# Kernel tuning notes

Hardware: AMD Instinct MI355X
Metric: run time of the kernel (lower is better)

Reference implementation:

```python
import jax, jax.numpy as jnp
import numpy as np

N_F, N_T = 211, 390
PAD_T, PAD_F = 2 * N_T, N_F  # zero_pad = (780, 211): right pad in time, bottom pad in freq
N_FILTS = 119
COCH_RESCALE = 100.0
CLAMP_MIN = 1e-8


def setup_inputs() -> dict:
    key = jax.random.key(0)
    k1, k2, k3 = jax.random.split(key, 3)
    x = jax.random.uniform(k1, (1, 1, N_F, N_T), dtype=jnp.float32)
    Ht_real = jax.random.normal(k2, (N_FILTS, N_F + PAD_F, N_T + PAD_T), dtype=jnp.float32)
    Ht_imag = jax.random.normal(k3, (N_FILTS, N_F + PAD_F, N_T + PAD_T), dtype=jnp.float32)
    return {"x": x, "Ht_real": Ht_real, "Ht_imag": Ht_imag}


def reference(x, Ht_real, Ht_imag):
    # x: [B, 1, N_F, N_T] cochleagram
    xs = x[:, 0] * COCH_RESCALE  # squeeze channel, rescale -> [B, N_F, N_T]
    # ConstantPad2d((0, PAD_T, 0, PAD_F)): pad time on the right, freq on the bottom
    xp = jnp.pad(xs, ((0, 0), (0, PAD_F), (0, PAD_T)))  # [B, 422, 1170]
    X = jnp.fft.fft2(xp)  # full (two-sided) 2D FFT, complex64
    H = Ht_real + 1j * Ht_imag  # [F, 422, 1170]
    Y = X[:, None, :, :] * H[None]  # broadcast complex multiply -> [B, F, 422, 1170]
    y = jnp.fft.ifft2(Y)
    real = jnp.real(y[:, :, :N_F, :N_T])  # crop to [B, F, 211, 390]
    power = jnp.clip(real * real, CLAMP_MIN)  # SquareReal with clamp min
    # AdaptiveAvgPool2d((1,1)) -> mean over freq/time, keep dims
    out = jnp.mean(power, axis=(-2, -1), keepdims=True)  # [B, F, 1, 1]
    return out
```

## Files before the change

kernel.cpp:

```cpp
#include <hip/hip_runtime.h>
#include <math.h>

constexpr int NF  = 119;
constexpr int D1  = 422;
constexpr int D2  = 1170;

constexpr int OFF_W390  = 0;
constexpr int OFF_T1170 = 390;
constexpr int OFF_W512  = 1560;
constexpr int OFF_CHIRP = 2072;
constexpr int OFF_U422  = 2283;
constexpr int OFF_BF    = 2494;
constexpr int OFF_T422  = 3006;

constexpr int KP1 = 2368;
constexpr int KB1 = KP1 * 2;
constexpr int ZS2 = 784;
constexpr int KP2 = 448;
constexpr int KB2 = KP2 * 2;

constexpr float SC_A   = 9.765625e-4f;
constexpr double S_D   = 1024.0 / (422.0 * 1170.0);
constexpr float TH_CL  = (float)(1e-8 / (S_D * S_D));
constexpr float FINAL  = (float)(S_D * S_D / (211.0 * 390.0));

typedef _Float16 h16;
typedef _Float16 h16x2 __attribute__((ext_vector_type(2)));
typedef _Float16 h16x8 __attribute__((ext_vector_type(8)));
typedef float f32x4 __attribute__((ext_vector_type(4)));

__device__ inline float2 cmul(float2 a, float2 b) {
  return make_float2(fmaf(a.x, b.x, -(a.y * b.y)), fmaf(a.x, b.y, a.y * b.x));
}
__device__ inline float2 cmulc(float2 a, float2 b) {
  return make_float2(fmaf(a.x, b.x, (a.y * b.y)), fmaf(a.y, b.x, -(a.x * b.y)));
}
__device__ inline void cfma(float2& c, float2 a, float2 b) {
  c.x = fmaf(a.x, b.x, fmaf(-a.y, b.y, c.x));
  c.y = fmaf(a.x, b.y, fmaf(a.y, b.x, c.y));
}

__device__ inline void async16(const void* g, void* l) {
  __builtin_amdgcn_global_load_lds((const __attribute__((address_space(1))) unsigned int*)g,
                                   (__attribute__((address_space(3))) unsigned int*)l, 16, 0, 0);
}

__device__ inline void fft512_lds(float2* a, const float2* w, int lt, int inv) {
  #pragma unroll
  for (int s = 0; s < 2; ++s) {
    int i = lt + (s << 8);
    int j = (int)(__brev((unsigned)i) >> 23);
    if (j > i) { float2 t = a[i]; a[i] = a[j]; a[j] = t; }
  }
  __syncthreads();
  for (int s = 1; s <= 9; ++s) {
    int half = 1 << (s - 1);
    int pos = lt & (half - 1);
    int grp = lt >> (s - 1);
    int i = (grp << s) + pos;
    int j = i + half;
    float2 tw = w[pos << (9 - s)];
    if (inv) tw.y = -tw.y;
    float2 t = cmul(a[j], tw);
    float2 ai = a[i];
    a[j] = make_float2(ai.x - t.x, ai.y - t.y);
    a[i] = make_float2(ai.x + t.x, ai.y + t.y);
    __syncthreads();
  }
}

__device__ inline void bluestein_core(float2* buf, const float2* w512s, const float2* __restrict__ Bt, int lt) {
  __syncthreads();
  fft512_lds(buf, w512s, lt, 0);
  #pragma unroll
  for (int s = 0; s < 2; ++s) { int i = lt + (s << 8); buf[i] = cmul(buf[i], Bt[i]); }
  __syncthreads();
  fft512_lds(buf, w512s, lt, 1);
}

template <int INV>
__device__ inline void dft390x3(const float2* a0, const float2* a1, const float2* a2,
                                float2* b0, float2* b1, float2* b2,
                                const float2* w, int tid,
                                float2& X0, float2& X1, float2& X2) {
  bool act = tid < 390;
  if (act) {
    int ka = tid % 30, nb = tid / 30;
    float2 c0 = make_float2(0.f, 0.f), c1 = c0, c2 = c0;
    int idx = 0, step = 13 * ka;
    #pragma unroll 6
    for (int na = 0; na < 30; ++na) {
      float2 tw = w[idx];
      if (INV) tw.y = -tw.y;
      int src = 13 * na + nb;
      cfma(c0, a0[src], tw);
      cfma(c1, a1[src], tw);
      cfma(c2, a2[src], tw);
      idx += step; if (idx >= 390) idx -= 390;
    }
    float2 t2 = w[nb * ka];
    if (INV) t2.y = -t2.y;
    int o = ka * 13 + nb;
    b0[o] = cmul(c0, t2);
    b1[o] = cmul(c1, t2);
    b2[o] = cmul(c2, t2);
  }
  __syncthreads();
  if (act) {
    int ka = tid % 30, kb = tid / 30;
    float2 c0 = make_float2(0.f, 0.f), c1 = c0, c2 = c0;
    int idx = 0, step = 30 * kb;
    #pragma unroll
    for (int nb = 0; nb < 13; ++nb) {
      float2 tw = w[idx];
      if (INV) tw.y = -tw.y;
      int src = ka * 13 + nb;
      cfma(c0, b0[src], tw);
      cfma(c1, b1[src], tw);
      cfma(c2, b2[src], tw);
      idx += step; if (idx >= 390) idx -= 390;
    }
    X0 = c0; X1 = c1; X2 = c2;
  }
  __syncthreads();
}


__global__ __launch_bounds__(512) void k_init(float2* __restrict__ tab, float* __restrict__ out) {
  int tid = threadIdx.x;
  __shared__ float2 bufE[512], bufO[512];
  __shared__ float2 w512s[512];
  __shared__ float2 chirps[211];
  const double PI = 3.14159265358979323846;
  for (int j = tid; j < 390; j += 512) {
    double a = -2.0 * PI * (double)j / 390.0; double s, c; sincos(a, &s, &c);
    tab[OFF_W390 + j] = make_float2((float)c, (float)s);
  }
  for (int j = tid; j < 1170; j += 512) {
    double a = 2.0 * PI * (double)j / 1170.0; double s, c; sincos(a, &s, &c);
    tab[OFF_T1170 + j] = make_float2((float)c, (float)s);
  }
  for (int j = tid; j < 422; j += 512) {
    double a = 2.0 * PI * (double)j / 422.0; double s, c; sincos(a, &s, &c);
    tab[OFF_T422 + j] = make_float2((float)c, (float)s);
  }
  for (int j = tid; j < 512; j += 512) {
    double a = -2.0 * PI * (double)j / 512.0; double s, c; sincos(a, &s, &c);
    float2 v = make_float2((float)c, (float)s);
    tab[OFF_W512 + j] = v; w512s[j] = v;
  }
  for (int n = tid; n < 211; n += 512) {
    int m = (n * n) % 422;
    double a = PI * (double)m / 211.0; double s, c; sincos(a, &s, &c);
    float2 v = make_float2((float)c, (float)s);
    tab[OFF_CHIRP + n] = v; chirps[n] = v;
  }
  for (int p = tid; p < 211; p += 512) {
    double a = 2.0 * PI * (double)p / 422.0; double s, c; sincos(a, &s, &c);
    tab[OFF_U422 + p] = make_float2((float)c, (float)s);
  }
  if (tid < NF) out[tid] = 0.0f;
  __syncthreads();
  int g = tid >> 8, lt = tid & 255;
  float2* buf = g ? bufO : bufE;
  #pragma unroll
  for (int s = 0; s < 2; ++s) {
    int i = lt + (s << 8);
    float2 v = make_float2(0.f, 0.f);
    if (i < 211) v = chirps[i];
    else if (i >= 302) v = chirps[512 - i];
    buf[i] = v;
  }
  __syncthreads();
  fft512_lds(buf, w512s, lt, 0);
  const float sc = 1.0f / 512.0f;
  if (g == 0) {
    #pragma unroll
    for (int s = 0; s < 2; ++s) {
      int i = lt + (s << 8);
      float2 v = buf[i];
      v.x *= sc; v.y *= sc;
      tab[OFF_BF + i] = v;
    }
  }
}

__global__ __launch_bounds__(256) void k_buildB(const float2* __restrict__ tab, h16* __restrict__ B1t) {
  int n = blockIdx.x;
  int q = n >> 1, c = n & 1;
  int tid = threadIdx.x;
  __shared__ float2 t[1170];
  for (int j = tid; j < 1170; j += 256) t[j] = tab[OFF_T1170 + j];
  __syncthreads();
  h16* row = B1t + (size_t)n * KP1;
  for (int k2 = tid; k2 < 1184; k2 += 256) {
    h16x2 h;
    if (k2 < 1170) {
      unsigned m = ((unsigned)q * (unsigned)k2) % 1170u;
      float2 e = t[m];
      h.x = (h16)(c ? e.y : e.x);
      h.y = (h16)(c ? e.x : -e.y);
    } else { h.x = (h16)0.f; h.y = (h16)0.f; }
    *(h16x2*)(row + 2 * k2) = h;
  }
}

__global__ __launch_bounds__(256) void k_buildA2(const float2* __restrict__ tab, h16* __restrict__ A2) {
  int p = blockIdx.x;
  int tid = threadIdx.x;
  __shared__ float2 t[422];
  for (int j = tid; j < 422; j += 256) t[j] = tab[OFF_T422 + j];
  __syncthreads();
  h16* row = A2 + (size_t)p * KP2;
  for (int k1 = tid; k1 < 224; k1 += 256) {
    h16x2 h; h.x = (h16)0.f; h.y = (h16)0.f;
    if (k1 < 212) {
      unsigned m = ((unsigned)p * (unsigned)k1) % 422u;
      float2 e = t[m];
      float cf = (k1 == 0 || k1 == 211) ? 1.f : 2.f;
      h.x = (h16)(cf * e.x);
      h.y = (h16)(-cf * e.y);
    }
    *(h16x2*)(row + 2 * k1) = h;
  }
}

__global__ __launch_bounds__(448) void k_rowfft(const float* __restrict__ x, const float2* __restrict__ tab,
                                                float2* __restrict__ X) {
  int i = blockIdx.x;
  int tid = threadIdx.x;
  __shared__ float2 a0[390], a1[390], a2[390], b0[390], b1[390], b2[390];
  __shared__ float2 w390s[390];
  __shared__ float2 t1170s[780];
  for (int j = tid; j < 390; j += 448) w390s[j] = tab[OFF_W390 + j];
  for (int j = tid; j < 780; j += 448) t1170s[j] = tab[OFF_T1170 + j];
  __syncthreads();
  for (int j = tid; j < 390; j += 448) {
    float xv = 100.0f * x[i * 390 + j];
    a0[j] = make_float2(xv, 0.0f);
    float2 t1 = t1170s[j];
    a1[j] = make_float2(xv * t1.x, -xv * t1.y);
    float2 t2 = t1170s[2 * j];
    a2[j] = make_float2(xv * t2.x, -xv * t2.y);
  }
  __syncthreads();
  float2 X0 = make_float2(0,0), X1 = X0, X2 = X0;
  dft390x3<0>(a0, a1, a2, b0, b1, b2, w390s, tid, X0, X1, X2);
  if (tid < 390) {
    size_t base = (size_t)i * D2 + 3 * (size_t)tid;
    X[base + 0] = X0; X[base + 1] = X1; X[base + 2] = X2;
  }
}

__global__ __launch_bounds__(512) void k_colfft(const float2* __restrict__ tab, float2* __restrict__ X) {
  int tid = threadIdx.x;
  int q0 = blockIdx.x * 8;
  int ncols = min(8, D2 - q0);
  __shared__ float Xre[8][212], Xim[8][212];
  __shared__ float2 bufE[512], bufO[512];
  __shared__ float2 w512s[512], chirps[211], u422s[211];
  for (int j = tid; j < 512; j += 512) w512s[j] = tab[OFF_W512 + j];
  for (int j = tid; j < 211; j += 512) { chirps[j] = tab[OFF_CHIRP + j]; u422s[j] = tab[OFF_U422 + j]; }
  const float2* Bf = tab + OFF_BF;
  for (int idx = tid; idx < 211 * 8; idx += 512) {
    int i = idx >> 3, c = idx & 7;
    float2 v = make_float2(0.f, 0.f);
    if (c < ncols) v = X[(size_t)i * D2 + q0 + c];
    Xre[c][i] = v.x; Xim[c][i] = v.y;
  }
  __syncthreads();
  int g = tid >> 8, lt = tid & 255;
  float2* buf = g ? bufO : bufE;
  for (int c = 0; c < ncols; ++c) {
    #pragma unroll
    for (int s = 0; s < 2; ++s) {
      int i2 = lt + (s << 8);
      float2 v = make_float2(0.f, 0.f);
      if (i2 < 211) {
        v = make_float2(Xre[c][i2], Xim[c][i2]);
        if (g) v = cmulc(v, u422s[i2]);
        v = cmulc(v, chirps[i2]);
      }
      buf[i2] = v;
    }
    bluestein_core(buf, w512s, Bf, lt);
    #pragma unroll
    for (int s = 0; s < 2; ++s) {
      int i2 = lt + (s << 8);
      if (i2 < 211) {
        float2 r = cmulc(buf[i2], chirps[i2]);
        X[(size_t)(2 * i2 + g) * D2 + q0 + c] = r;
      }
    }
    __syncthreads();
  }
}

__global__ __launch_bounds__(256) void k_buildA(const float* __restrict__ Hr, const float* __restrict__ Hi,
                                                const float2* __restrict__ X, h16* __restrict__ A, int f0) {
  int k1 = blockIdx.x, fl = blockIdx.y, f = f0 + fl;
  int tid = threadIdx.x;
  int m1 = (422 - k1) % 422;
  size_t hb  = (size_t)f * (D1 * D2) + (size_t)k1 * D2;
  size_t hmb = (size_t)f * (D1 * D2) + (size_t)m1 * D2;
  const float2* Xr = X + (size_t)k1 * D2;
  h16* Arow = A + ((size_t)fl * 212 + k1) * KP1;
  for (int k2 = tid; k2 < 1170; k2 += 256) {
    int rk = k2 ? 1170 - k2 : 0;
    float gr = 0.5f * (Hr[hb + k2] + Hr[hmb + rk]);
    float gi = 0.5f * (Hi[hb + k2] - Hi[hmb + rk]);
    float2 xv = Xr[k2];
    float yr = (xv.x * gr - xv.y * gi) * SC_A;
    float yi = (xv.x * gi + xv.y * gr) * SC_A;
    h16x2 h; h.x = (h16)yr; h.y = (h16)yi;
    *(h16x2*)(Arow + 2 * k2) = h;
  }
  if (tid < 28) Arow[2340 + tid] = (h16)0.f;
}

__global__ __launch_bounds__(256) void k_gemm1(const h16* __restrict__ A, const h16* __restrict__ B1t,
                                               h16* __restrict__ Z) {
  int fl = blockIdx.y;
  int mt = blockIdx.x / 7, nt = blockIdx.x % 7;
  const int M0 = mt ? 84 : 0;
  const int N0 = (nt == 6) ? 652 : nt * 128;
  int tid = threadIdx.x, wv = tid >> 6, ln = tid & 63;
  int l15 = ln & 15, l16 = ln >> 4;
  int wm = (wv >> 1) * 64, wn = (wv & 1) * 64;
  __shared__ __align__(16) h16 Alds[128 * 32];
  __shared__ __align__(16) h16 Blds[128 * 32];
  const char* Ag = (const char*)(A + (size_t)fl * 212 * KP1);
  const char* Bg = (const char*)B1t;
  f32x4 acc[4][4] = {};
  for (int kc = 0; kc < 74; ++kc) {
    int kb = kc * 64;
    __syncthreads();
    #pragma unroll
    for (int s = 0; s < 2; ++s) {
      int L = ((wv * 2 + s) * 64 + ln) * 16;
      int row = L >> 6, colb = L & 63;
      async16(Ag + (size_t)(M0 + row) * KB1 + kb + colb, (char*)Alds + (wv * 2 + s) * 1024);
      async16(Bg + (size_t)(N0 + row) * KB1 + kb + colb, (char*)Blds + (wv * 2 + s) * 1024);
    }
    __syncthreads();
    h16x8 af[4], bf[4];
    const h16x8* Av = (const h16x8*)Alds;
    const h16x8* Bv = (const h16x8*)Blds;
    #pragma unroll
    for (int i = 0; i < 4; ++i) af[i] = Av[(wm + i * 16 + l15) * 4 + l16];
    #pragma unroll
    for (int j = 0; j < 4; ++j) bf[j] = Bv[(wn + j * 16 + l15) * 4 + l16];
    #pragma unroll
    for (int i = 0; i < 4; ++i)
      #pragma unroll
      for (int j = 0; j < 4; ++j)
        acc[i][j] = __builtin_amdgcn_mfma_f32_16x16x32_f16(af[i], bf[j], acc[i][j], 0, 0, 0);
  }
  h16* Zf = Z + (size_t)fl * 212 * ZS2;
  #pragma unroll
  for (int i = 0; i < 4; ++i) {
    #pragma unroll
    for (int j = 0; j < 4; ++j) {
      #pragma unroll
      for (int r = 0; r < 4; ++r) {
        int m = M0 + wm + i * 16 + l16 * 4 + r;
        int n = N0 + wn + j * 16 + l15;
        Zf[(size_t)m * ZS2 + n] = (h16)acc[i][j][r];
      }
    }
  }
}

__global__ __launch_bounds__(256) void k_gemm2(const h16* __restrict__ A2, const h16* __restrict__ Z,
                                               float* __restrict__ out, int f0) {
  int fl = blockIdx.y, f = f0 + fl;
  int mt = blockIdx.x / 7, nt = blockIdx.x % 7;
  const int M0 = (mt == 3) ? 147 : mt * 64;
  const int pmin = (mt == 3) ? 192 : 0;
  const int N0 = (nt == 6) ? 326 : nt * 64;
  const int qmin = (nt == 6) ? 384 : 0;
  int tid = threadIdx.x, wv = tid >> 6, ln = tid & 63;
  int l15 = ln & 15, l16 = ln >> 4;
  int wm = (wv >> 1) * 32, wn = (wv & 1) * 32;
  __shared__ __align__(16) h16 Alds[64 * 32];
  __shared__ __align__(16) h16 Blds[64 * 32];
  const char* Ag = (const char*)A2;
  const h16* Zf = Z + (size_t)fl * 212 * ZS2;
  f32x4 acc[2][2] = {};
  int brow = tid >> 4, bseg = tid & 15;
  for (int kc = 0; kc < 14; ++kc) {
    __syncthreads();
    {
      int L = (wv * 64 + ln) * 16;
      int row = L >> 6, colb = L & 63;
      async16(Ag + (size_t)(M0 + row) * KB2 + kc * 64 + colb, (char*)Alds + wv * 1024);
    }
    {
      int k1r = kc * 16 + brow;
      uint2 u0 = make_uint2(0, 0), u1 = make_uint2(0, 0);
      if (k1r < 212) {
        const uint2* src = (const uint2*)(Zf + (size_t)k1r * ZS2 + 2 * N0 + bseg * 8);
        u0 = src[0]; u1 = src[1];
      }
      unsigned int w[4] = {u0.x, u0.y, u1.x, u1.y};
      unsigned short* Bs = (unsigned short*)Blds;
      #pragma unroll
      for (int h = 0; h < 4; ++h) {
        int qh = bseg * 4 + h;
        Bs[qh * 32 + 2 * brow + 0] = (unsigned short)(w[h] & 0xffffu);
        Bs[qh * 32 + 2 * brow + 1] = (unsigned short)(w[h] >> 16);
      }
    }
    __syncthreads();
    h16x8 af[2], bf[2];
    const h16x8* Av = (const h16x8*)Alds;
    const h16x8* Bv = (const h16x8*)Blds;
    af[0] = Av[(wm + l15) * 4 + l16];
    af[1] = Av[(wm + 16 + l15) * 4 + l16];
    bf[0] = Bv[(wn + l15) * 4 + l16];
    bf[1] = Bv[(wn + 16 + l15) * 4 + l16];
    #pragma unroll
    for (int i = 0; i < 2; ++i)
      #pragma unroll
      for (int j = 0; j < 2; ++j)
        acc[i][j] = __builtin_amdgcn_mfma_f32_16x16x32_f16(af[i], bf[j], acc[i][j], 0, 0, 0);
  }
  float accs = 0.f;
  #pragma unroll
  for (int i = 0; i < 2; ++i) {
    #pragma unroll
    for (int j = 0; j < 2; ++j) {
      #pragma unroll
      for (int r = 0; r < 4; ++r) {
        int p = M0 + wm + i * 16 + l16 * 4 + r;
        int q = N0 + wn + j * 16 + l15;
        if (p >= pmin && q >= qmin) {
          float y = acc[i][j][r];
          accs += fmaxf(y * y, TH_CL);
        }
      }
    }
  }
  for (int off = 32; off > 0; off >>= 1) accs += __shfl_down(accs, off, 64);
  __shared__ float wred[4];
  if (ln == 0) wred[wv] = accs;
  __syncthreads();
  if (tid == 0) atomicAdd(&out[f], (wred[0] + wred[1] + wred[2] + wred[3]) * FINAL);
}

extern "C" void kernel_launch(void* const* d_in, const int* in_sizes, int n_in,
                              void* d_out, int out_size, void* d_ws, size_t ws_size,
                              hipStream_t stream) {
  const float* x  = (const float*)d_in[0];
  const float* Hr = (const float*)d_in[1];
  const float* Hi = (const float*)d_in[2];
  float* out = (float*)d_out;
  char* base = (char*)d_ws;

  size_t off = 0;
  auto alloc = [&](size_t bytes) { size_t cur = off; off = (off + bytes + 255) & ~(size_t)255; return cur; };
  float2* tab = (float2*)(base + alloc(32768));
  float2* X   = (float2*)(base + alloc((size_t)D1 * D2 * sizeof(float2)));
  h16* B1t    = (h16*)(base + alloc((size_t)780 * KP1 * 2));
  h16* A2     = (h16*)(base + alloc((size_t)211 * KP2 * 2));
  size_t perA = (size_t)212 * KP1 * 2;
  size_t perZ = (size_t)212 * ZS2 * 2;
  long long avail = (long long)ws_size - (long long)off - 512;
  int chunk = (avail > 0) ? (int)(avail / (long long)(perA + perZ)) : 1;
  if (chunk < 1) chunk = 1;
  if (chunk > NF) chunk = NF;
  h16* A = (h16*)(base + alloc(perA * chunk));
  h16* Zp = (h16*)(base + alloc(perZ * chunk));

  k_init<<<dim3(1), dim3(512), 0, stream>>>(tab, out);
  k_buildB<<<dim3(780), dim3(256), 0, stream>>>(tab, B1t);
  k_buildA2<<<dim3(211), dim3(256), 0, stream>>>(tab, A2);
  k_rowfft<<<dim3(211), dim3(448), 0, stream>>>(x, tab, X);
  k_colfft<<<dim3(147), dim3(512), 0, stream>>>(tab, X);
  for (int f0 = 0; f0 < NF; f0 += chunk) {
    int nf = NF - f0;
    if (nf > chunk) nf = chunk;
    k_buildA<<<dim3(212, nf), dim3(256), 0, stream>>>(Hr, Hi, X, A, f0);
    k_gemm1<<<dim3(14, nf), dim3(256), 0, stream>>>(A, B1t, Zp);
    k_gemm2<<<dim3(28, nf), dim3(256), 0, stream>>>(A2, Zp, out, f0);
  }
}
```

Before: 779.8 us.

## Transpose intermediate Z layout, deepen gemm1 K-tile, and enlarge gemm2 tiles

gemm1 now writes its output transposed (rows indexed by output column pair, with real and imaginary halves split along K) and stages 128-wide K chunks per iteration, halving the number of barriers. gemm2 can therefore stream its B operand with async 16-byte loads instead of a manual per-element LDS transpose. It also covers the full 256-row M dimension with 512 threads and 4 N tiles, and A2 is rebuilt as a padded 256x448 real-valued K layout. Both GEMMs use a 1D grid that interleaves 8 filters per group, which is likely aimed at L2 reuse of the shared B1t/A2 operands. The cost is more LDS per block and some wasted MFMA work on the padded rows.

```diff
diff --git a/kernel.cpp b/kernel.cpp
--- a/kernel.cpp
+++ b/kernel.cpp
@@ -15,9 +15,9 @@
 
 constexpr int KP1 = 2368;
 constexpr int KB1 = KP1 * 2;
-constexpr int ZS2 = 784;
 constexpr int KP2 = 448;
 constexpr int KB2 = KP2 * 2;
+constexpr int ZROW = 448;
 
 constexpr float SC_A   = 9.765625e-4f;
 constexpr double S_D   = 1024.0 / (422.0 * 1170.0);
@@ -212,16 +212,16 @@
   for (int j = tid; j < 422; j += 256) t[j] = tab[OFF_T422 + j];
   __syncthreads();
   h16* row = A2 + (size_t)p * KP2;
-  for (int k1 = tid; k1 < 224; k1 += 256) {
-    h16x2 h; h.x = (h16)0.f; h.y = (h16)0.f;
-    if (k1 < 212) {
-      unsigned m = ((unsigned)p * (unsigned)k1) % 422u;
+  for (int k = tid; k < KP2; k += 256) {
+    int c = k / 224, k1 = k - c * 224;
+    float v = 0.f;
+    if (p < 211 && k1 < 212) {
+      int m = (p * k1) % 422;
       float2 e = t[m];
       float cf = (k1 == 0 || k1 == 211) ? 1.f : 2.f;
-      h.x = (h16)(cf * e.x);
-      h.y = (h16)(-cf * e.y);
-    }
-    *(h16x2*)(row + 2 * k1) = h;
+      v = c ? (-cf * e.y) : (cf * e.x);
+    }
+    row[k] = (h16)v;
   }
 }
 
@@ -319,34 +319,106 @@
 }
 
 __global__ __launch_bounds__(256) void k_gemm1(const h16* __restrict__ A, const h16* __restrict__ B1t,
-                                               h16* __restrict__ Z) {
-  int fl = blockIdx.y;
-  int mt = blockIdx.x / 7, nt = blockIdx.x % 7;
+                                               h16* __restrict__ Z2, int nf) {
+  int id = blockIdx.x;
+  int r8 = id & 7;
+  int t14 = (id >> 3) % 14;
+  int g8 = (id >> 3) / 14;
+  int fl = r8 + (g8 << 3);
+  if (fl >= nf) return;
+  int mt = t14 / 7, nt = t14 % 7;
   const int M0 = mt ? 84 : 0;
   const int N0 = (nt == 6) ? 652 : nt * 128;
   int tid = threadIdx.x, wv = tid >> 6, ln = tid & 63;
   int l15 = ln & 15, l16 = ln >> 4;
   int wm = (wv >> 1) * 64, wn = (wv & 1) * 64;
-  __shared__ __align__(16) h16 Alds[128 * 32];
-  __shared__ __align__(16) h16 Blds[128 * 32];
+  __shared__ __align__(16) h16 Alds[128 * 64];
+  __shared__ __align__(16) h16 Blds[128 * 64];
   const char* Ag = (const char*)(A + (size_t)fl * 212 * KP1);
   const char* Bg = (const char*)B1t;
   f32x4 acc[4][4] = {};
-  for (int kc = 0; kc < 74; ++kc) {
-    int kb = kc * 64;
-    __syncthreads();
-    #pragma unroll
-    for (int s = 0; s < 2; ++s) {
-      int L = ((wv * 2 + s) * 64 + ln) * 16;
-      int row = L >> 6, colb = L & 63;
-      async16(Ag + (size_t)(M0 + row) * KB1 + kb + colb, (char*)Alds + (wv * 2 + s) * 1024);
-      async16(Bg + (size_t)(N0 + row) * KB1 + kb + colb, (char*)Blds + (wv * 2 + s) * 1024);
-    }
-    __syncthreads();
-    h16x8 af[4], bf[4];
+  for (int kc = 0; kc < 37; ++kc) {
+    int kb = kc * 128;
+    __syncthreads();
+    #pragma unroll
+    for (int s = 0; s < 4; ++s) {
+      int idx = s * 256 + tid;
+      int row = idx >> 3, colb = (idx & 7) * 16;
+      async16(Ag + (size_t)(M0 + row) * KB1 + kb + colb, (char*)Alds + idx * 16);
+      async16(Bg + (size_t)(N0 + row) * KB1 + kb + colb, (char*)Blds + idx * 16);
+    }
+    __syncthreads();
     const h16x8* Av = (const h16x8*)Alds;
     const h16x8* Bv = (const h16x8*)Blds;
     #pragma unroll
+    for (int h = 0; h < 2; ++h) {
+      h16x8 af[4], bf[4];
+      #pragma unroll
+      for (int i = 0; i < 4; ++i) af[i] = Av[(wm + i * 16 + l15) * 8 + (h << 2) + l16];
+      #pragma unroll
+      for (int j = 0; j < 4; ++j) bf[j] = Bv[(wn + j * 16 + l15) * 8 + (h << 2) + l16];
+      #pragma unroll
+      for (int i = 0; i < 4; ++i)
+        #pragma unroll
+        for (int j = 0; j < 4; ++j)
+          acc[i][j] = __builtin_amdgcn_mfma_f32_16x16x32_f16(af[i], bf[j], acc[i][j], 0, 0, 0);
+    }
+  }
+  h16* Zf = Z2 + (size_t)fl * 390 * ZROW;
+  #pragma unroll
+  for (int i = 0; i < 4; ++i) {
+    #pragma unroll
+    for (int j = 0; j < 4; ++j) {
+      #pragma unroll
+      for (int r = 0; r < 4; ++r) {
+        int m = M0 + wm + i * 16 + l16 * 4 + r;
+        if (m < 212) {
+          int n = N0 + wn + j * 16 + l15;
+          int q = n >> 1, c = n & 1;
+          Zf[(size_t)q * ZROW + c * 224 + m] = (h16)acc[i][j][r];
+        }
+      }
+    }
+  }
+}
+
+__global__ __launch_bounds__(512) void k_gemm2(const h16* __restrict__ A2, const h16* __restrict__ Z2,
+                                               float* __restrict__ out, int f0, int nf) {
+  int id = blockIdx.x;
+  int r8 = id & 7;
+  int nt = (id >> 3) & 3;
+  int g8 = (id >> 3) >> 2;
+  int fl = r8 + (g8 << 3);
+  if (fl >= nf) return;
+  int f = f0 + fl;
+  const int N0 = (nt == 3) ? 262 : nt * 128;
+  const int qmin = (nt == 3) ? 384 : 0;
+  int tid = threadIdx.x, wv = tid >> 6, ln = tid & 63;
+  int l15 = ln & 15, l16 = ln >> 4;
+  int wm = (wv >> 1) * 64, wn = (wv & 1) * 64;
+  __shared__ __align__(16) h16 Alds[256 * 32];
+  __shared__ __align__(16) h16 Blds[128 * 32];
+  const char* Ag = (const char*)A2;
+  const char* Bg = (const char*)(Z2 + (size_t)fl * 390 * ZROW);
+  f32x4 acc[4][4] = {};
+  for (int kc = 0; kc < 14; ++kc) {
+    int kb = kc * 64;
+    __syncthreads();
+    #pragma unroll
+    for (int s = 0; s < 2; ++s) {
+      int idx = s * 512 + tid;
+      int row = idx >> 2, colb = (idx & 3) * 16;
+      async16(Ag + (size_t)row * KB2 + kb + colb, (char*)Alds + idx * 16);
+    }
+    {
+      int row = tid >> 2, colb = (tid & 3) * 16;
+      async16(Bg + (size_t)(N0 + row) * KB2 + kb + colb, (char*)Blds + tid * 16);
+    }
+    __syncthreads();
+    const h16x8* Av = (const h16x8*)Alds;
+    const h16x8* Bv = (const h16x8*)Blds;
+    h16x8 af[4], bf[4];
+    #pragma unroll
     for (int i = 0; i < 4; ++i) af[i] = Av[(wm + i * 16 + l15) * 4 + l16];
     #pragma unroll
     for (int j = 0; j < 4; ++j) bf[j] = Bv[(wn + j * 16 + l15) * 4 + l16];
@@ -356,85 +428,16 @@
       for (int j = 0; j < 4; ++j)
         acc[i][j] = __builtin_amdgcn_mfma_f32_16x16x32_f16(af[i], bf[j], acc[i][j], 0, 0, 0);
   }
-  h16* Zf = Z + (size_t)fl * 212 * ZS2;
+  float accs = 0.f;
   #pragma unroll
   for (int i = 0; i < 4; ++i) {
     #pragma unroll
     for (int j = 0; j < 4; ++j) {
       #pragma unroll
       for (int r = 0; r < 4; ++r) {
-        int m = M0 + wm + i * 16 + l16 * 4 + r;
-        int n = N0 + wn + j * 16 + l15;
-        Zf[(size_t)m * ZS2 + n] = (h16)acc[i][j][r];
-      }
-    }
-  }
-}
-
-__global__ __launch_bounds__(256) void k_gemm2(const h16* __restrict__ A2, const h16* __restrict__ Z,
-                                               float* __restrict__ out, int f0) {
-  int fl = blockIdx.y, f = f0 + fl;
-  int mt = blockIdx.x / 7, nt = blockIdx.x % 7;
-  const int M0 = (mt == 3) ? 147 : mt * 64;
-  const int pmin = (mt == 3) ? 192 : 0;
-  const int N0 = (nt == 6) ? 326 : nt * 64;
-  const int qmin = (nt == 6) ? 384 : 0;
-  int tid = threadIdx.x, wv = tid >> 6, ln = tid & 63;
-  int l15 = ln & 15, l16 = ln >> 4;
-  int wm = (wv >> 1) * 32, wn = (wv & 1) * 32;
-  __shared__ __align__(16) h16 Alds[64 * 32];
-  __shared__ __align__(16) h16 Blds[64 * 32];
-  const char* Ag = (const char*)A2;
-  const h16* Zf = Z + (size_t)fl * 212 * ZS2;
-  f32x4 acc[2][2] = {};
-  int brow = tid >> 4, bseg = tid & 15;
-  for (int kc = 0; kc < 14; ++kc) {
-    __syncthreads();
-    {
-      int L = (wv * 64 + ln) * 16;
-      int row = L >> 6, colb = L & 63;
-      async16(Ag + (size_t)(M0 + row) * KB2 + kc * 64 + colb, (char*)Alds + wv * 1024);
-    }
-    {
-      int k1r = kc * 16 + brow;
-      uint2 u0 = make_uint2(0, 0), u1 = make_uint2(0, 0);
-      if (k1r < 212) {
-        const uint2* src = (const uint2*)(Zf + (size_t)k1r * ZS2 + 2 * N0 + bseg * 8);
-        u0 = src[0]; u1 = src[1];
-      }
-      unsigned int w[4] = {u0.x, u0.y, u1.x, u1.y};
-      unsigned short* Bs = (unsigned short*)Blds;
-      #pragma unroll
-      for (int h = 0; h < 4; ++h) {
-        int qh = bseg * 4 + h;
-        Bs[qh * 32 + 2 * brow + 0] = (unsigned short)(w[h] & 0xffffu);
-        Bs[qh * 32 + 2 * brow + 1] = (unsigned short)(w[h] >> 16);
-      }
-    }
-    __syncthreads();
-    h16x8 af[2], bf[2];
-    const h16x8* Av = (const h16x8*)Alds;
-    const h16x8* Bv = (const h16x8*)Blds;
-    af[0] = Av[(wm + l15) * 4 + l16];
-    af[1] = Av[(wm + 16 + l15) * 4 + l16];
-    bf[0] = Bv[(wn + l15) * 4 + l16];
-    bf[1] = Bv[(wn + 16 + l15) * 4 + l16];
-    #pragma unroll
-    for (int i = 0; i < 2; ++i)
-      #pragma unroll
-      for (int j = 0; j < 2; ++j)
-        acc[i][j] = __builtin_amdgcn_mfma_f32_16x16x32_f16(af[i], bf[j], acc[i][j], 0, 0, 0);
-  }
-  float accs = 0.f;
-  #pragma unroll
-  for (int i = 0; i < 2; ++i) {
-    #pragma unroll
-    for (int j = 0; j < 2; ++j) {
-      #pragma unroll
-      for (int r = 0; r < 4; ++r) {
-        int p = M0 + wm + i * 16 + l16 * 4 + r;
+        int p = wm + i * 16 + l16 * 4 + r;
         int q = N0 + wn + j * 16 + l15;
-        if (p >= pmin && q >= qmin) {
+        if (p < 211 && q < 390 && q >= qmin) {
           float y = acc[i][j][r];
           accs += fmaxf(y * y, TH_CL);
         }
@@ -442,10 +445,15 @@
     }
   }
   for (int off = 32; off > 0; off >>= 1) accs += __shfl_down(accs, off, 64);
-  __shared__ float wred[4];
+  __shared__ float wred[8];
   if (ln == 0) wred[wv] = accs;
   __syncthreads();
-  if (tid == 0) atomicAdd(&out[f], (wred[0] + wred[1] + wred[2] + wred[3]) * FINAL);
+  if (tid == 0) {
+    float tot = 0.f;
+    #pragma unroll
+    for (int w = 0; w < 8; ++w) tot += wred[w];
+    atomicAdd(&out[f], tot * FINAL);
+  }
 }
 
 extern "C" void kernel_launch(void* const* d_in, const int* in_sizes, int n_in,
@@ -462,26 +470,27 @@
   float2* tab = (float2*)(base + alloc(32768));
   float2* X   = (float2*)(base + alloc((size_t)D1 * D2 * sizeof(float2)));
   h16* B1t    = (h16*)(base + alloc((size_t)780 * KP1 * 2));
-  h16* A2     = (h16*)(base + alloc((size_t)211 * KP2 * 2));
+  h16* A2     = (h16*)(base + alloc((size_t)256 * KP2 * 2));
   size_t perA = (size_t)212 * KP1 * 2;
-  size_t perZ = (size_t)212 * ZS2 * 2;
+  size_t perZ = (size_t)390 * ZROW * 2;
   long long avail = (long long)ws_size - (long long)off - 512;
   int chunk = (avail > 0) ? (int)(avail / (long long)(perA + perZ)) : 1;
   if (chunk < 1) chunk = 1;
   if (chunk > NF) chunk = NF;
-  h16* A = (h16*)(base + alloc(perA * chunk));
+  h16* A  = (h16*)(base + alloc(perA * chunk));
   h16* Zp = (h16*)(base + alloc(perZ * chunk));
 
   k_init<<<dim3(1), dim3(512), 0, stream>>>(tab, out);
   k_buildB<<<dim3(780), dim3(256), 0, stream>>>(tab, B1t);
-  k_buildA2<<<dim3(211), dim3(256), 0, stream>>>(tab, A2);
+  k_buildA2<<<dim3(256), dim3(256), 0, stream>>>(tab, A2);
   k_rowfft<<<dim3(211), dim3(448), 0, stream>>>(x, tab, X);
   k_colfft<<<dim3(147), dim3(512), 0, stream>>>(tab, X);
   for (int f0 = 0; f0 < NF; f0 += chunk) {
     int nf = NF - f0;
     if (nf > chunk) nf = chunk;
+    int ngrp = (nf + 7) / 8;
     k_buildA<<<dim3(212, nf), dim3(256), 0, stream>>>(Hr, Hi, X, A, f0);
-    k_gemm1<<<dim3(14, nf), dim3(256), 0, stream>>>(A, B1t, Zp);
-    k_gemm2<<<dim3(28, nf), dim3(256), 0, stream>>>(A2, Zp, out, f0);
-  }
-}
+    k_gemm1<<<dim3(8 * 14 * ngrp), dim3(256), 0, stream>>>(A, B1t, Zp, nf);
+    k_gemm2<<<dim3(8 * 4 * ngrp), dim3(512), 0, stream>>>(A2, Zp, out, f0, nf);
+  }
+}
```

Result: slower. 807.8 us (+3.6%).
